# Kernel tuning notes

Hardware: AMD Instinct MI355X
Metric: run time of the kernel (lower is better)

The kernel has to match this reference:

```python
import jax, jax.numpy as jnp
import numpy as np

EPS = 1e-05
DECAY = 0.99
K = 2048   # codebook_size
D = 256    # codebook_dim


def setup_inputs() -> dict:
    key = jax.random.key(0)
    k1, k2, k3 = jax.random.split(key, 3)
    hidden_states = jax.random.normal(k1, (16, 4096, D), dtype=jnp.float32)
    embed_sum = jax.random.normal(k2, (K, D), dtype=jnp.float32)
    cluster_usage = jax.random.uniform(k3, (K,), dtype=jnp.float32)
    return {"hidden_states": hidden_states, "embed_sum": embed_sum, "cluster_usage": cluster_usage}


def reference(hidden_states, embed_sum, cluster_usage):
    # embed property: embed_sum / clamp(cluster_usage, min=eps)
    embed = embed_sum / jnp.clip(cluster_usage, EPS, None)[:, None]  # [K, D]

    shape = hidden_states.shape
    flat = hidden_states.reshape(-1, shape[-1])  # [N, D]

    # quantize: cdist(p=2) + argmin. argmin over squared distances is identical
    # to argmin over euclidean distances, avoiding the sqrt.
    x2 = jnp.sum(flat * flat, axis=-1, keepdims=True)          # [N, 1]
    e2 = jnp.sum(embed * embed, axis=-1)[None, :]              # [1, K]
    d2 = x2 - 2.0 * (flat @ embed.T) + e2                      # [N, K]
    flat_ind = jnp.argmin(d2, axis=-1)                         # [N]

    embed_ind = flat_ind.reshape(shape[:-1])                   # [B, T]
    quantize = embed[flat_ind].reshape(shape)                  # [B, T, D]

    # training-path EMA accumulation (scatter_add -> segment_sum), functional form
    counts = jax.ops.segment_sum(jnp.ones_like(flat_ind, dtype=flat.dtype), flat_ind, num_segments=K)
    sums = jax.ops.segment_sum(flat, flat_ind, num_segments=K)  # [K, D]
    new_cluster_usage = cluster_usage * DECAY + counts * (1.0 - DECAY)
    new_embed_sum = embed_sum * DECAY + sums * (1.0 - DECAY)

    return quantize, embed_ind, new_cluster_usage, new_embed_sum
```

## Files before the change

kernel.cpp:

```cpp
#include <hip/hip_runtime.h>

#define EPSF 1e-5f
#define DECAYF 0.99f
#define KCODES 2048
#define DIM 256

typedef _Float16 f16;
typedef f16 f16x8 __attribute__((ext_vector_type(8)));
typedef float f32x4 __attribute__((ext_vector_type(4)));

#define MFMA16(A, B, C) __builtin_amdgcn_mfma_f32_16x16x32_f16(A, B, C, 0, 0, 0)

#define OFF_AH 0
#define OFF_AL 16384
#define OFF_BH 32768
#define OFF_BL 49152

__device__ __forceinline__ void gload_lds16(const void* g, void* l) {
    __builtin_amdgcn_global_load_lds(
        (const __attribute__((address_space(1))) void*)g,
        (__attribute__((address_space(3))) void*)l, 16, 0, 0);
}

__global__ __launch_bounds__(256) void split_prep_kernel(
    const float* __restrict__ x, f16* __restrict__ xh, f16* __restrict__ xl, int nsplit,
    const float* __restrict__ embed_sum, const float* __restrict__ usage,
    float* __restrict__ embed, f16* __restrict__ eh, f16* __restrict__ el,
    float* __restrict__ e2, unsigned* __restrict__ pmax, unsigned* __restrict__ pmin,
    float* __restrict__ sums, int* __restrict__ cnt)
{
    if ((int)blockIdx.x < nsplit) {
        int i = blockIdx.x * 256 + threadIdx.x;
        f32x4 v0 = ((const f32x4*)x)[2 * i];
        f32x4 v1 = ((const f32x4*)x)[2 * i + 1];
        f16x8 h, l;
        float p = 0.f;
        #pragma unroll
        for (int t = 0; t < 4; ++t) {
            f16 h0 = (f16)v0[t]; h[t] = h0; l[t] = (f16)(v0[t] - (float)h0);
            f16 h1 = (f16)v1[t]; h[t + 4] = h1; l[t + 4] = (f16)(v1[t] - (float)h1);
            p += v0[t] * v0[t] + v1[t] * v1[t];
        }
        ((f16x8*)xh)[i] = h;
        ((f16x8*)xl)[i] = l;
        #pragma unroll
        for (int m = 1; m <= 16; m <<= 1) p += __shfl_xor(p, m, 64);
        float q = fmaxf(p, __shfl_xor(p, 32, 64));
        __shared__ float wmax[4];
        if ((threadIdx.x & 63) == 0) wmax[threadIdx.x >> 6] = q;
        __syncthreads();
        if (threadIdx.x == 0) {
            float bm = fmaxf(fmaxf(wmax[0], wmax[1]), fmaxf(wmax[2], wmax[3]));
            atomicMax(&pmax[blockIdx.x & 63], __float_as_uint(bm) | 0x80000000u);
        }
    } else if ((int)blockIdx.x < nsplit + KCODES) {
        int k = blockIdx.x - nsplit;
        int d = threadIdx.x;
        float inv = 1.0f / fmaxf(usage[k], EPSF);
        float e = embed_sum[k * DIM + d] * inv;
        embed[k * DIM + d] = e;
        float ec = fminf(fmaxf(e, -65000.0f), 65000.0f);
        f16 h = (f16)ec;
        f16 l = (f16)(ec - (float)h);
        eh[k * DIM + d] = h;
        el[k * DIM + d] = l;
        float sq = e * e;
        #pragma unroll
        for (int off = 32; off > 0; off >>= 1) sq += __shfl_down(sq, off, 64);
        __shared__ float ws[4];
        if ((threadIdx.x & 63) == 0) ws[threadIdx.x >> 6] = sq;
        __syncthreads();
        if (threadIdx.x == 0) {
            float s = ws[0] + ws[1] + ws[2] + ws[3];
            e2[k] = s;
            atomicMax(&pmin[k & 63], ~__float_as_uint(-s));
        }
    } else {
        int k = blockIdx.x - nsplit - KCODES;
        sums[k * DIM + threadIdx.x] = 0.f;
        if (threadIdx.x == 0) cnt[k] = 0;
    }
}

__global__ __launch_bounds__(256) void compactA_kernel(
    const float* __restrict__ e2, const unsigned* __restrict__ pmax,
    const unsigned* __restrict__ pmin, float* __restrict__ ce2,
    int* __restrict__ cmap, int* __restrict__ meta)
{
    __shared__ int ps[256];
    __shared__ float sT;
    const int t = threadIdx.x;
    if (t < 64) {
        unsigned km = pmax[t], kn = pmin[t];
        #pragma unroll
        for (int m = 1; m <= 32; m <<= 1) {
            km = max(km, (unsigned)__shfl_xor((int)km, m, 64));
            kn = max(kn, (unsigned)__shfl_xor((int)kn, m, 64));
        }
        if (t == 0) {
            float mx = __uint_as_float(km & 0x7FFFFFFFu);
            float mn = -__uint_as_float(~kn);
            float T0 = 2.0f * sqrtf(mx) + sqrtf(mn);
            sT = T0 * T0 * 1.0002f + 1.0f;
        }
    }
    __syncthreads();
    const float T = sT;
    int flag[8], pre[8], s = 0;
    float ev[8];
    #pragma unroll
    for (int j = 0; j < 8; ++j) {
        ev[j] = e2[t * 8 + j];
        flag[j] = (ev[j] <= T) ? 1 : 0;
        pre[j] = s; s += flag[j];
    }
    ps[t] = s;
    __syncthreads();
    for (int off = 1; off < 256; off <<= 1) {
        int v = (t >= off) ? ps[t - off] : 0;
        __syncthreads();
        ps[t] += v;
        __syncthreads();
    }
    const int ex = (t > 0) ? ps[t - 1] : 0;
    const int kp = ps[255];
    #pragma unroll
    for (int j = 0; j < 8; ++j) {
        const int k = t * 8 + j;
        if (flag[j]) {
            const int p = ex + pre[j];
            ce2[p] = ev[j];
            cmap[p] = k;
        }
    }
    for (int j = t; j < KCODES; j += 256)
        if (j >= kp) { ce2[j] = 3.4e38f; cmap[j] = 0; }
    if (t == 0) { meta[0] = kp; meta[1] = (kp + 255) & ~255; }
}

__global__ __launch_bounds__(512, 2) void argmin_kernel(
    const f16* __restrict__ xh, const f16* __restrict__ xl,
    const f16* __restrict__ eh, const f16* __restrict__ el,
    const float* __restrict__ ce2, const int* __restrict__ cmap,
    const int* __restrict__ meta, int* __restrict__ flat_ind, int* __restrict__ cnt)
{
    __shared__ __align__(1024) char lds[2 * 65536 + 8192];
    float* e2s = (float*)(lds + 131072);

    const int ncc = meta[1] >> 5;
    const int tid  = threadIdx.x;
    const int w    = tid >> 6, lane = tid & 63;
    const int l15  = lane & 15, l4 = lane >> 4;
    const int wm   = w >> 1, wn = w & 1;
    const int row0 = blockIdx.x * 256;
    const int gsw  = (lane & 3) ^ ((lane >> 3) & 3);
    const int lq   = lane >> 2;
    const int rslot = (l4 ^ ((l15 >> 1) & 3)) * 16;

    f32x4 acc[4][8];
    float best[16];
    int   bidx[16];
    #pragma unroll
    for (int t = 0; t < 16; ++t) { best[t] = 3.4e38f; bidx[t] = 0; }

    auto stageA = [&](const f16* rowbase, int koff, char* unit) {
        #pragma unroll
        for (int q = 0; q < 2; ++q) {
            const int r = w * 32 + q * 16 + lq;
            gload_lds16(rowbase + (size_t)r * DIM + koff + gsw * 8,
                        unit + w * 2048 + q * 1024 + lane * 16);
        }
    };
    auto stageB = [&](int tileBase, int koff, char* unitH, char* unitL) {
        #pragma unroll
        for (int q = 0; q < 2; ++q) {
            const int r = w * 32 + q * 16 + lq;
            const int pr = cmap[tileBase + r];
            gload_lds16(eh + (size_t)pr * DIM + koff + gsw * 8,
                        unitH + w * 2048 + q * 1024 + lane * 16);
            gload_lds16(el + (size_t)pr * DIM + koff + gsw * 8,
                        unitL + w * 2048 + q * 1024 + lane * 16);
        }
    };

    ((f32x4*)e2s)[tid] = ((const f32x4*)ce2)[tid];
    stageA(xh + (size_t)row0 * DIM, 0, lds + OFF_AH);
    stageA(xl + (size_t)row0 * DIM, 0, lds + OFF_AL);
    stageB(0, 0, lds + OFF_BH, lds + OFF_BL);

    for (int cc = 0; cc < ncc; ++cc) {
        char* buf  = lds + (cc & 1) * 65536;
        char* nbuf = lds + ((cc + 1) & 1) * 65536;
        const int ct = cc >> 3, sd = cc & 7;
        const int nn = cc + 1;
        const int nct = nn >> 3, nsd = nn & 7;
        const bool more = (nn < ncc);

        if (sd == 0) {
            #pragma unroll
            for (int i = 0; i < 4; ++i)
                #pragma unroll
                for (int j = 0; j < 8; ++j)
                    acc[i][j] = (f32x4){0.f, 0.f, 0.f, 0.f};
        }

        asm volatile("s_waitcnt vmcnt(0)" ::: "memory");
        __builtin_amdgcn_s_barrier();
        __builtin_amdgcn_sched_barrier(0);

        f16x8 ah[4], al[4], bh[8], bl[8];
        #pragma unroll
        for (int i = 0; i < 4; ++i)
            ah[i] = *(const f16x8*)(buf + OFF_AH + (wm * 64 + i * 16 + l15) * 64 + rslot);
        #pragma unroll
        for (int j = 0; j < 8; ++j)
            bh[j] = *(const f16x8*)(buf + OFF_BH + (wn * 128 + j * 16 + l15) * 64 + rslot);
        __builtin_amdgcn_sched_barrier(0);

        if (more) {
            stageA(xh + (size_t)row0 * DIM, nsd * 32, nbuf + OFF_AH);
            stageA(xl + (size_t)row0 * DIM, nsd * 32, nbuf + OFF_AL);
            stageB(nct * 256, nsd * 32, nbuf + OFF_BH, nbuf + OFF_BL);
        }

        #pragma unroll
        for (int i = 0; i < 4; ++i)
            #pragma unroll
            for (int j = 0; j < 8; ++j)
                acc[i][j] = MFMA16(ah[i], bh[j], acc[i][j]);

        #pragma unroll
        for (int i = 0; i < 4; ++i)
            al[i] = *(const f16x8*)(buf + OFF_AL + (wm * 64 + i * 16 + l15) * 64 + rslot);
        #pragma unroll
        for (int i = 0; i < 4; ++i)
            #pragma unroll
            for (int j = 0; j < 8; ++j)
                acc[i][j] = MFMA16(al[i], bh[j], acc[i][j]);

        #pragma unroll
        for (int j = 0; j < 8; ++j)
            bl[j] = *(const f16x8*)(buf + OFF_BL + (wn * 128 + j * 16 + l15) * 64 + rslot);
        #pragma unroll
        for (int i = 0; i < 4; ++i)
            #pragma unroll
            for (int j = 0; j < 8; ++j)
                acc[i][j] = MFMA16(ah[i], bl[j], acc[i][j]);

        if (sd == 7) {
            const int cbase = ct * 256 + wn * 128;
            #pragma unroll
            for (int j = 0; j < 8; ++j) {
                const int col = cbase + j * 16 + l15;
                const float e2v = e2s[col];
                #pragma unroll
                for (int i = 0; i < 4; ++i)
                    #pragma unroll
                    for (int r = 0; r < 4; ++r) {
                        float m = fmaf(-2.0f, acc[i][j][r], e2v);
                        const int tt_ = i * 4 + r;
                        if (m < best[tt_]) { best[tt_] = m; bidx[tt_] = col; }
                    }
            }
        }
    }

    __syncthreads();
    float* rv = (float*)lds;
    int*   ri = (int*)(lds + 4096);
    #pragma unroll
    for (int tt_ = 0; tt_ < 16; ++tt_) {
        float v = best[tt_];
        int  ix = bidx[tt_];
        #pragma unroll
        for (int m = 1; m <= 8; m <<= 1) {
            float ov = __shfl_xor(v, m, 64);
            int  oix = __shfl_xor(ix, m, 64);
            if (ov < v || (ov == v && oix < ix)) { v = ov; ix = oix; }
        }
        if (l15 == 0) {
            const int rl = wm * 64 + (tt_ >> 2) * 16 + l4 * 4 + (tt_ & 3);
            rv[rl * 2 + wn] = v;
            ri[rl * 2 + wn] = ix;
        }
    }
    __syncthreads();
    if (tid < 256) {
        float v0 = rv[tid * 2], v1 = rv[tid * 2 + 1];
        int   i0 = ri[tid * 2], i1 = ri[tid * 2 + 1];
        int ibc = (v1 < v0 || (v1 == v0 && i1 < i0)) ? i1 : i0;
        int ib = cmap[ibc];
        flat_ind[row0 + tid] = ib;
        unsigned long long pending = ~0ULL;
        while (pending) {
            int leader = __ffsll((long long)pending) - 1;
            int lind = __shfl(ib, leader, 64);
            unsigned long long same = __ballot(ib == lind);
            if ((tid & 63) == leader) atomicAdd(&cnt[lind], (int)__popcll(same));
            pending &= ~same;
        }
    }
}

__global__ __launch_bounds__(256) void scan_kernel(
    const int* __restrict__ cnt, int* __restrict__ offs, int* __restrict__ cursor)
{
    __shared__ int ps[256];
    const int t = threadIdx.x;
    int pre[8], s = 0;
    #pragma unroll
    for (int j = 0; j < 8; ++j) { pre[j] = s; s += cnt[t * 8 + j]; }
    ps[t] = s;
    __syncthreads();
    for (int off = 1; off < 256; off <<= 1) {
        int v = (t >= off) ? ps[t - off] : 0;
        __syncthreads();
        ps[t] += v;
        __syncthreads();
    }
    int ex = (t > 0) ? ps[t - 1] : 0;
    #pragma unroll
    for (int j = 0; j < 8; ++j) {
        offs[t * 8 + j]   = ex + pre[j];
        cursor[t * 8 + j] = ex + pre[j];
    }
}

__global__ __launch_bounds__(256) void assign_kernel(
    const int* __restrict__ flat_ind, int* __restrict__ cursor,
    int* __restrict__ rowlist, int* __restrict__ codesorted)
{
    const int i    = blockIdx.x * 256 + threadIdx.x;
    const int lane = threadIdx.x & 63;
    const int ind  = flat_ind[i];
    int pos = 0;
    unsigned long long pending = ~0ULL;
    while (pending) {
        int leader = __ffsll((long long)pending) - 1;
        int lind = __shfl(ind, leader, 64);
        unsigned long long same = __ballot(ind == lind);
        if (ind == lind) {
            int base = 0;
            if (lane == leader) base = atomicAdd(&cursor[lind], (int)__popcll(same));
            base = __shfl(base, leader, 64);
            pos = base + (int)__popcll(same & ((1ULL << lane) - 1ULL));
        }
        pending &= ~same;
    }
    rowlist[pos] = i;
    codesorted[pos] = ind;
}

__global__ __launch_bounds__(256) void codesum_quant_kernel(
    const float* __restrict__ x, const int* __restrict__ rowlist,
    const int* __restrict__ codesorted, float* __restrict__ sums, int nc,
    const float* __restrict__ embed, const int* __restrict__ flat_ind,
    float* __restrict__ out_q, float* __restrict__ out_ind_f, int N)
{
    if ((int)blockIdx.x < nc) {
        const int p0 = blockIdx.x * 64;
        __shared__ int rows[64], codes[64];
        if (threadIdx.x < 64) {
            rows[threadIdx.x]  = rowlist[p0 + threadIdx.x];
            codes[threadIdx.x] = codesorted[p0 + threadIdx.x];
        }
        __syncthreads();
        const int d = threadIdx.x;
        float acc = 0.f;
        int cur = codes[0];
        #pragma unroll 4
        for (int r = 0; r < 64; ++r) {
            const int c = codes[r];
            if (c != cur) {
                atomicAdd(&sums[(size_t)cur * DIM + d], acc);
                acc = 0.f; cur = c;
            }
            acc += x[(size_t)rows[r] * DIM + d];
        }
        atomicAdd(&sums[(size_t)cur * DIM + d], acc);
    } else {
        int i = (blockIdx.x - nc) * 256 + threadIdx.x;
        int row = i >> 6, c4 = i & 63;
        int ind = flat_ind[row];
        ((f32x4*)out_q)[i] = ((const f32x4*)embed)[ind * 64 + c4];
        if (i < N) out_ind_f[i] = (float)flat_ind[i];
    }
}

__global__ __launch_bounds__(256) void finalize_kernel(
    const float* __restrict__ embed_sum, const float* __restrict__ usage,
    const float* __restrict__ sums, const int* __restrict__ cnt,
    float* __restrict__ out_usage, float* __restrict__ out_es)
{
    const int k = blockIdx.x, d = threadIdx.x;
    out_es[k * DIM + d] = embed_sum[k * DIM + d] * DECAYF + sums[k * DIM + d] * (1.0f - DECAYF);
    if (d == 0)
        out_usage[k] = usage[k] * DECAYF + (float)cnt[k] * (1.0f - DECAYF);
}

extern "C" void kernel_launch(void* const* d_in, const int* in_sizes, int n_in,
                              void* d_out, int out_size, void* d_ws, size_t ws_size,
                              hipStream_t stream)
{
    const float* hs        = (const float*)d_in[0];
    const float* embed_sum = (const float*)d_in[1];
    const float* usage     = (const float*)d_in[2];
    const int N = in_sizes[0] / DIM;

    float* ws_f      = (float*)d_ws;
    float* embed     = ws_f;
    float* e2        = embed + KCODES * DIM;
    float* sums      = e2 + KCODES;
    int*   cnt       = (int*)(sums + KCODES * DIM);
    unsigned* pmax   = (unsigned*)(cnt + KCODES);
    unsigned* pmin   = pmax + 64;
    f16*   eh        = (f16*)(pmin + 64);
    f16*   el        = eh + KCODES * DIM;
    float* ce2       = (float*)(el + KCODES * DIM);
    int*   cmap      = (int*)(ce2 + KCODES);
    int*   meta      = cmap + KCODES;
    int*   offs      = meta + 16;
    int*   cursor    = offs + KCODES;
    int*   rowlist   = cursor + KCODES;
    int*   codesorted= rowlist + N;
    int*   flat_ind  = codesorted + N;

    float* out_q     = (float*)d_out;
    float* out_ind   = out_q + (size_t)N * DIM;
    float* out_usage = out_ind + N;
    float* out_es    = out_usage + KCODES;

    f16* xh = (f16*)out_q;
    f16* xl = xh + (size_t)N * DIM;

    hipMemsetAsync(pmax, 0, 128 * sizeof(unsigned), stream);

    const int nsplit = N * DIM / 8 / 256;
    split_prep_kernel<<<nsplit + 2 * KCODES, 256, 0, stream>>>(
        hs, xh, xl, nsplit, embed_sum, usage, embed, eh, el, e2, pmax, pmin,
        sums, cnt);
    compactA_kernel<<<1, 256, 0, stream>>>(e2, pmax, pmin, ce2, cmap, meta);
    argmin_kernel<<<N / 256, 512, 0, stream>>>(xh, xl, eh, el, ce2, cmap, meta,
                                               flat_ind, cnt);
    scan_kernel<<<1, 256, 0, stream>>>(cnt, offs, cursor);
    assign_kernel<<<N / 256, 256, 0, stream>>>(flat_ind, cursor, rowlist, codesorted);
    const int nc = N / 64;
    const int nq = N * DIM / 4 / 256;
    codesum_quant_kernel<<<nc + nq, 256, 0, stream>>>(
        hs, rowlist, codesorted, sums, nc, embed, flat_ind, out_q, out_ind, N);
    finalize_kernel<<<KCODES, 256, 0, stream>>>(embed_sum, usage, sums, cnt,
                                                out_usage, out_es);
}
```

Baseline: 267.5 us.

## Tighten codebook pruning threshold using per-row distance to eight smallest-norm codes

Splits prep into an embed-only prep kernel, a single-block kernel that picks the eight codes with the smallest squared norm, and a split kernel that also computes each row's exact distance to those eight candidates. The pruning threshold becomes the max over rows of (|x| + sqrt(dmin))^2 instead of (2·max|x| + min|e|)^2, so fewer codes survive compaction and the argmin GEMM covers fewer codes. In exchange it adds two kernel launches and per-row dot-product work in the split pass, and it serialises the embed prep before the x split.

New measurement: 263.9 us. Within noise of the previous version (-1.3%).

```diff
diff --git a/kernel.cpp b/kernel.cpp
--- a/kernel.cpp
+++ b/kernel.cpp
@@ -22,39 +22,13 @@
         (__attribute__((address_space(3))) void*)l, 16, 0, 0);
 }
 
-__global__ __launch_bounds__(256) void split_prep_kernel(
-    const float* __restrict__ x, f16* __restrict__ xh, f16* __restrict__ xl, int nsplit,
+__global__ __launch_bounds__(256) void prep_kernel(
     const float* __restrict__ embed_sum, const float* __restrict__ usage,
     float* __restrict__ embed, f16* __restrict__ eh, f16* __restrict__ el,
-    float* __restrict__ e2, unsigned* __restrict__ pmax, unsigned* __restrict__ pmin,
-    float* __restrict__ sums, int* __restrict__ cnt)
-{
-    if ((int)blockIdx.x < nsplit) {
-        int i = blockIdx.x * 256 + threadIdx.x;
-        f32x4 v0 = ((const f32x4*)x)[2 * i];
-        f32x4 v1 = ((const f32x4*)x)[2 * i + 1];
-        f16x8 h, l;
-        float p = 0.f;
-        #pragma unroll
-        for (int t = 0; t < 4; ++t) {
-            f16 h0 = (f16)v0[t]; h[t] = h0; l[t] = (f16)(v0[t] - (float)h0);
-            f16 h1 = (f16)v1[t]; h[t + 4] = h1; l[t + 4] = (f16)(v1[t] - (float)h1);
-            p += v0[t] * v0[t] + v1[t] * v1[t];
-        }
-        ((f16x8*)xh)[i] = h;
-        ((f16x8*)xl)[i] = l;
-        #pragma unroll
-        for (int m = 1; m <= 16; m <<= 1) p += __shfl_xor(p, m, 64);
-        float q = fmaxf(p, __shfl_xor(p, 32, 64));
-        __shared__ float wmax[4];
-        if ((threadIdx.x & 63) == 0) wmax[threadIdx.x >> 6] = q;
-        __syncthreads();
-        if (threadIdx.x == 0) {
-            float bm = fmaxf(fmaxf(wmax[0], wmax[1]), fmaxf(wmax[2], wmax[3]));
-            atomicMax(&pmax[blockIdx.x & 63], __float_as_uint(bm) | 0x80000000u);
-        }
-    } else if ((int)blockIdx.x < nsplit + KCODES) {
-        int k = blockIdx.x - nsplit;
+    float* __restrict__ e2, float* __restrict__ sums, int* __restrict__ cnt)
+{
+    if ((int)blockIdx.x < KCODES) {
+        int k = blockIdx.x;
         int d = threadIdx.x;
         float inv = 1.0f / fmaxf(usage[k], EPSF);
         float e = embed_sum[k * DIM + d] * inv;
@@ -70,38 +44,127 @@
         __shared__ float ws[4];
         if ((threadIdx.x & 63) == 0) ws[threadIdx.x >> 6] = sq;
         __syncthreads();
-        if (threadIdx.x == 0) {
-            float s = ws[0] + ws[1] + ws[2] + ws[3];
-            e2[k] = s;
-            atomicMax(&pmin[k & 63], ~__float_as_uint(-s));
-        }
+        if (threadIdx.x == 0) e2[k] = ws[0] + ws[1] + ws[2] + ws[3];
     } else {
-        int k = blockIdx.x - nsplit - KCODES;
+        int k = blockIdx.x - KCODES;
         sums[k * DIM + threadIdx.x] = 0.f;
         if (threadIdx.x == 0) cnt[k] = 0;
     }
 }
 
+__global__ __launch_bounds__(256) void pick_kernel(
+    const float* __restrict__ e2, int* __restrict__ cidx, float* __restrict__ e2c)
+{
+    __shared__ unsigned long long red[256];
+    const int t = threadIdx.x;
+    unsigned long long local[8];
+    #pragma unroll
+    for (int j = 0; j < 8; ++j) {
+        float v = e2[t * 8 + j];
+        local[j] = ((unsigned long long)__float_as_uint(v) << 32) | (unsigned)(t * 8 + j);
+    }
+    for (int r = 0; r < 8; ++r) {
+        unsigned long long m = ~0ULL;
+        #pragma unroll
+        for (int j = 0; j < 8; ++j) m = (local[j] < m) ? local[j] : m;
+        red[t] = m;
+        __syncthreads();
+        for (int off = 128; off > 0; off >>= 1) {
+            if (t < off) red[t] = (red[t + off] < red[t]) ? red[t + off] : red[t];
+            __syncthreads();
+        }
+        unsigned long long g = red[0];
+        __syncthreads();
+        int k = (int)(g & 0xFFFFFFFFu);
+        if (t == 0) { cidx[r] = k; e2c[r] = __uint_as_float((unsigned)(g >> 32)); }
+        #pragma unroll
+        for (int j = 0; j < 8; ++j)
+            if ((int)(local[j] & 0xFFFFFFFFu) == k) local[j] = ~0ULL;
+    }
+}
+
+__global__ __launch_bounds__(256) void splitx_kernel(
+    const float* __restrict__ x, f16* __restrict__ xh, f16* __restrict__ xl,
+    const float* __restrict__ embed, const int* __restrict__ cidx,
+    const float* __restrict__ e2c, unsigned* __restrict__ pmax)
+{
+    __shared__ float ecs[8 * 256];
+    __shared__ float e2cs[8];
+    __shared__ float wmax[4];
+    const int t = threadIdx.x;
+    #pragma unroll
+    for (int j = 0; j < 8; ++j) {
+        int idx = t * 8 + j;
+        ecs[idx] = embed[(size_t)cidx[idx >> 8] * DIM + (idx & 255)];
+    }
+    if (t < 8) e2cs[t] = e2c[t];
+    __syncthreads();
+
+    int i = blockIdx.x * 256 + t;
+    f32x4 v0 = ((const f32x4*)x)[2 * i];
+    f32x4 v1 = ((const f32x4*)x)[2 * i + 1];
+    float xv[8];
+    #pragma unroll
+    for (int q = 0; q < 4; ++q) { xv[q] = v0[q]; xv[q + 4] = v1[q]; }
+    f16x8 h, l;
+    float p = 0.f;
+    #pragma unroll
+    for (int j = 0; j < 8; ++j) {
+        f16 hh = (f16)xv[j]; h[j] = hh; l[j] = (f16)(xv[j] - (float)hh);
+        p += xv[j] * xv[j];
+    }
+    ((f16x8*)xh)[i] = h;
+    ((f16x8*)xl)[i] = l;
+
+    const int base = (t & 31) * 8;
+    float dot[8];
+    #pragma unroll
+    for (int r = 0; r < 8; ++r) {
+        const float* er = &ecs[r * 256 + base];
+        float d = 0.f;
+        #pragma unroll
+        for (int j = 0; j < 8; ++j) d = fmaf(xv[j], er[j], d);
+        dot[r] = d;
+    }
+    #pragma unroll
+    for (int m = 1; m <= 16; m <<= 1) {
+        p += __shfl_xor(p, m, 64);
+        #pragma unroll
+        for (int r = 0; r < 8; ++r) dot[r] += __shfl_xor(dot[r], m, 64);
+    }
+    float dmin2 = 3.4e38f;
+    #pragma unroll
+    for (int r = 0; r < 8; ++r) {
+        float d2 = fmaxf(fmaf(-2.f, dot[r], p) + e2cs[r], 0.f);
+        dmin2 = fminf(dmin2, d2);
+    }
+    float key = sqrtf(p) + sqrtf(dmin2);
+    key = key * key;
+    #pragma unroll
+    for (int m = 1; m <= 32; m <<= 1) key = fmaxf(key, __shfl_xor(key, m, 64));
+    if ((t & 63) == 0) wmax[t >> 6] = key;
+    __syncthreads();
+    if (t == 0) {
+        float bm = fmaxf(fmaxf(wmax[0], wmax[1]), fmaxf(wmax[2], wmax[3]));
+        atomicMax(&pmax[blockIdx.x & 63], __float_as_uint(bm) | 0x80000000u);
+    }
+}
+
 __global__ __launch_bounds__(256) void compactA_kernel(
     const float* __restrict__ e2, const unsigned* __restrict__ pmax,
-    const unsigned* __restrict__ pmin, float* __restrict__ ce2,
-    int* __restrict__ cmap, int* __restrict__ meta)
+    float* __restrict__ ce2, int* __restrict__ cmap, int* __restrict__ meta)
 {
     __shared__ int ps[256];
     __shared__ float sT;
     const int t = threadIdx.x;
     if (t < 64) {
-        unsigned km = pmax[t], kn = pmin[t];
-        #pragma unroll
-        for (int m = 1; m <= 32; m <<= 1) {
+        unsigned km = pmax[t];
+        #pragma unroll
+        for (int m = 1; m <= 32; m <<= 1)
             km = max(km, (unsigned)__shfl_xor((int)km, m, 64));
-            kn = max(kn, (unsigned)__shfl_xor((int)kn, m, 64));
-        }
         if (t == 0) {
             float mx = __uint_as_float(km & 0x7FFFFFFFu);
-            float mn = -__uint_as_float(~kn);
-            float T0 = 2.0f * sqrtf(mx) + sqrtf(mn);
-            sT = T0 * T0 * 1.0002f + 1.0f;
+            sT = mx * 1.0005f + 1.0f;
         }
     }
     __syncthreads();
@@ -413,8 +476,9 @@
     float* sums      = e2 + KCODES;
     int*   cnt       = (int*)(sums + KCODES * DIM);
     unsigned* pmax   = (unsigned*)(cnt + KCODES);
-    unsigned* pmin   = pmax + 64;
-    f16*   eh        = (f16*)(pmin + 64);
+    int*   cidx      = (int*)(pmax + 64);
+    float* e2c       = (float*)(cidx + 8);
+    f16*   eh        = (f16*)(e2c + 8);
     f16*   el        = eh + KCODES * DIM;
     float* ce2       = (float*)(el + KCODES * DIM);
     int*   cmap      = (int*)(ce2 + KCODES);
@@ -433,13 +497,14 @@
     f16* xh = (f16*)out_q;
     f16* xl = xh + (size_t)N * DIM;
 
-    hipMemsetAsync(pmax, 0, 128 * sizeof(unsigned), stream);
-
+    hipMemsetAsync(pmax, 0, 64 * sizeof(unsigned), stream);
+
+    prep_kernel<<<2 * KCODES, 256, 0, stream>>>(embed_sum, usage, embed, eh, el, e2,
+                                                sums, cnt);
+    pick_kernel<<<1, 256, 0, stream>>>(e2, cidx, e2c);
     const int nsplit = N * DIM / 8 / 256;
-    split_prep_kernel<<<nsplit + 2 * KCODES, 256, 0, stream>>>(
-        hs, xh, xl, nsplit, embed_sum, usage, embed, eh, el, e2, pmax, pmin,
-        sums, cnt);
-    compactA_kernel<<<1, 256, 0, stream>>>(e2, pmax, pmin, ce2, cmap, meta);
+    splitx_kernel<<<nsplit, 256, 0, stream>>>(hs, xh, xl, embed, cidx, e2c, pmax);
+    compactA_kernel<<<1, 256, 0, stream>>>(e2, pmax, ce2, cmap, meta);
     argmin_kernel<<<N / 256, 512, 0, stream>>>(xh, xl, eh, el, ce2, cmap, meta,
                                                flat_ind, cnt);
     scan_kernel<<<1, 256, 0, stream>>>(cnt, offs, cursor);
```
